# Kernel tuning notes

Hardware: AMD Instinct MI355X
Metric: run time of the kernel (lower is better)

## Reference

```python
import jax, jax.numpy as jnp
import numpy as np

PAD_IDX = 0

def _gru_layer(xs, W_ih, W_hh, b_ih, b_hh):
    # xs: [B, S, D]; W_ih: [3H, D]; W_hh: [3H, H]
    B = xs.shape[0]
    H = W_hh.shape[1]
    # precompute input-side gate projections for all timesteps: [S, B, 3H]
    xg = jnp.einsum('bsd,gd->sbg', xs, W_ih) + b_ih

    def step(h, xg_t):
        hg = h @ W_hh.T + b_hh                      # [B, 3H]
        xr, xz, xn = jnp.split(xg_t, 3, axis=-1)
        hr, hz, hn = jnp.split(hg, 3, axis=-1)
        r = jax.nn.sigmoid(xr + hr)
        z = jax.nn.sigmoid(xz + hz)
        n = jnp.tanh(xn + r * hn)
        h_new = (1.0 - z) * n + z * h
        return h_new, h_new

    h0 = jnp.zeros((B, H), dtype=xs.dtype)
    _, ys = jax.lax.scan(step, h0, xg)              # ys: [S, B, H]
    return jnp.transpose(ys, (1, 0, 2))             # [B, S, H]

def setup_inputs() -> dict:
    key = jax.random.key(0)
    ks = jax.random.split(key, 12)
    V, E, H = 32000, 256, 512
    B, S = 64, 512
    s_e = 1.0 / np.sqrt(H)
    inp = {
        'x': jax.random.randint(ks[0], (B, S), 0, V, dtype=jnp.int32),
        'emb': jax.random.normal(ks[1], (V, E), dtype=jnp.float32),
        'W_ih0': jax.random.uniform(ks[2], (3 * H, E), jnp.float32, -s_e, s_e),
        'W_hh0': jax.random.uniform(ks[3], (3 * H, H), jnp.float32, -s_e, s_e),
        'b_ih0': jax.random.uniform(ks[4], (3 * H,), jnp.float32, -s_e, s_e),
        'b_hh0': jax.random.uniform(ks[5], (3 * H,), jnp.float32, -s_e, s_e),
        'W_ih1': jax.random.uniform(ks[6], (3 * H, H), jnp.float32, -s_e, s_e),
        'W_hh1': jax.random.uniform(ks[7], (3 * H, H), jnp.float32, -s_e, s_e),
        'b_ih1': jax.random.uniform(ks[8], (3 * H,), jnp.float32, -s_e, s_e),
        'b_hh1': jax.random.uniform(ks[9], (3 * H,), jnp.float32, -s_e, s_e),
        'W_fc': jax.random.uniform(ks[10], (1, H), jnp.float32, -s_e, s_e),
        'b_fc': jax.random.uniform(ks[11], (1,), jnp.float32, -s_e, s_e),
    }
    return inp

def reference(x, emb, W_ih0, W_hh0, b_ih0, b_hh0, W_ih1, W_hh1, b_ih1, b_hh1, W_fc, b_fc):
    # embedding with padding_idx: pad row is zero
    emb_z = emb.at[PAD_IDX].set(0.0)
    h = emb_z[x]                                    # [B, S, E]
    h = _gru_layer(h, W_ih0, W_hh0, b_ih0, b_hh0)   # [B, S, H]
    h = _gru_layer(h, W_ih1, W_hh1, b_ih1, b_hh1)   # [B, S, H]
    final = h[:, -1, :]                             # [B, H]
    return jax.nn.sigmoid(final @ W_fc.T + b_fc)    # [B, 1]
```

## Files before the change

### kernel.cpp

```cpp
#include <hip/hip_runtime.h>
#include <math.h>

typedef short  s8v __attribute__((ext_vector_type(8)));
typedef float  f4v __attribute__((ext_vector_type(4)));
typedef unsigned long long ull;

#define S_LEN 512
#define BATCH 64
#define HID   512
#define TPB   256

#define WI0H_OFF 0L
#define WI0L_OFF 786432L
#define WH0H_OFF 1572864L
#define WH0L_OFF 3145728L
#define WI1H_OFF 4718592L
#define WI1L_OFF 6291456L
#define WH1H_OFF 7864320L
#define WH1L_OFF 9437184L
#define XEB_OFF  11010048L
#define H0R_OFF  27787264L
#define H1R_OFF  94896128L
#define NEED_FAST 95420416L

#define BAR_BYTES   4096
#define HBUF_BYTES  (HID*BATCH*4)
#define A_OFF       BAR_BYTES
#define B_OFF       (A_OFF + 2*HBUF_BYTES)
#define XE_OFF      (B_OFF + 2*HBUF_BYTES)
#define XE_BYTES    ((size_t)S_LEN*64*BATCH*16)

__device__ __forceinline__ float fexp2(float x){ return __builtin_amdgcn_exp2f(x); }
__device__ __forceinline__ float frcp (float x){ return __builtin_amdgcn_rcpf(x); }
__device__ __forceinline__ float sigm (float x){ return frcp(1.f + fexp2(-1.44269504089f*x)); }
__device__ __forceinline__ float tanhx(float x){ return 1.f - 2.f*frcp(1.f + fexp2(2.88539008178f*x)); }
__device__ __forceinline__ float sigmoid_f(float v){ return 1.0f/(1.0f + expf(-v)); }

__device__ __forceinline__ unsigned short f2bf(float f){
  unsigned int u = __float_as_uint(f);
  u = u + 0x7FFFu + ((u >> 16) & 1u);
  return (unsigned short)(u >> 16);
}
__device__ __forceinline__ float bf2f(unsigned short s){
  return __uint_as_float(((unsigned int)s) << 16);
}

__global__ void wcvt_kernel(const float* __restrict__ Wih0, const float* __restrict__ Whh0,
                            const float* __restrict__ Wih1, const float* __restrict__ Whh1,
                            char* __restrict__ ws)
{
  int idx = blockIdx.x * TPB + threadIdx.x;
  const float* src; long hi_off, lo_off; int pos;
  if (idx < 393216)       { src = Wih0; pos = idx;           hi_off = WI0H_OFF; lo_off = WI0L_OFF; }
  else if (idx < 1179648) { src = Whh0; pos = idx - 393216;  hi_off = WH0H_OFF; lo_off = WH0L_OFF; }
  else if (idx < 1966080) { src = Wih1; pos = idx - 1179648; hi_off = WI1H_OFF; lo_off = WI1L_OFF; }
  else                    { src = Whh1; pos = idx - 1966080; hi_off = WH1H_OFF; lo_off = WH1L_OFF; }
  float w = src[pos];
  unsigned short h = f2bf(w);
  unsigned short l = f2bf(w - bf2f(h));
  ((unsigned short*)(ws + hi_off))[pos] = h;
  ((unsigned short*)(ws + lo_off))[pos] = l;
}

__global__ void gather_xe_bf_kernel(const int* __restrict__ x,
                                    const float* __restrict__ emb,
                                    char* __restrict__ ws)
{
  int idx = blockIdx.x * TPB + threadIdx.x;
  int k4 = idx & 63;
  int n  = idx >> 6;
  int t = n >> 6, b = n & 63;
  int tok = x[b * S_LEN + t];
  float4 v = make_float4(0.f,0.f,0.f,0.f);
  if (tok != 0) v = ((const float4*)emb)[(size_t)tok * 64 + k4];
  unsigned int lo = (unsigned int)f2bf(v.x) | ((unsigned int)f2bf(v.y) << 16);
  unsigned int hi = (unsigned int)f2bf(v.z) | ((unsigned int)f2bf(v.w) << 16);
  ((uint2*)(ws + XEB_OFF))[(long)n * 64 + k4] = make_uint2(lo, hi);
}

__device__ __forceinline__ void st_rec(ull* p, ull v){
  __hip_atomic_store(p, v, __ATOMIC_RELAXED, __HIP_MEMORY_SCOPE_AGENT);
}

template<int NKS>
__device__ __forceinline__ void load_ct(const ull* __restrict__ sl, int b,
                                        int quad, int k0s, unsigned want,
                                        s8v* __restrict__ bf)
{
  ull d[NKS][4];
  for (;;){
    #pragma unroll
    for (int ks = 0; ks < NKS; ++ks){
      const int e = k0s + ks*4 + quad;
      const ull* p = sl + (long)(4*e)*64 + b;
      #pragma unroll
      for (int i = 0; i < 4; ++i)
        d[ks][i] = __hip_atomic_load(p + (long)i*64, __ATOMIC_RELAXED, __HIP_MEMORY_SCOPE_AGENT);
    }
    bool ok = true;
    #pragma unroll
    for (int ks = 0; ks < NKS; ++ks)
      #pragma unroll
      for (int i = 0; i < 4; ++i)
        ok = ok && ((unsigned)(d[ks][i] >> 32) == want);
    if (__all(ok)) break;
    __builtin_amdgcn_s_sleep(1);
  }
  #pragma unroll
  for (int ks = 0; ks < NKS; ++ks){
    s8v v;
    #pragma unroll
    for (int i = 0; i < 4; ++i){
      unsigned lo = (unsigned)d[ks][i];
      v[2*i]   = (short)(lo & 0xFFFFu);
      v[2*i+1] = (short)(lo >> 16);
    }
    bf[ks] = v;
  }
}

template<int NKS, int ROLE>
__device__ __forceinline__ void scan_body(
    int isL1, int rowWG, int bh, int wave, int lane, int tid, int j0, int b0,
    const s8v* __restrict__ Whi, const s8v* __restrict__ Wlo, int AKs, int k0s,
    const s8v* __restrict__ xsrc,
    const ull* __restrict__ rsrc, int slotMask,
    const float* __restrict__ bih, const float* __restrict__ bhh,
    ull* __restrict__ rout, int outMask,
    f4v* __restrict__ part)
{
  const int quad = lane >> 4, col = lane & 15;

  s8v ahi[3][NKS], alo[3][NKS];
  #pragma unroll
  for (int rt = 0; rt < 3; ++rt){
    const int row = rt*512 + j0 + col;
    #pragma unroll
    for (int ks = 0; ks < NKS; ++ks){
      const int e = row*AKs + k0s + ks*4 + quad;
      ahi[rt][ks] = Whi[e];
      alo[rt][ks] = Wlo[e];
    }
  }

  float cr[4], cz[4], cnx[4], cnh[4], hp[4];
  #pragma unroll
  for (int r4 = 0; r4 < 4; ++r4){
    int j = j0 + wave*4 + r4;
    cr[r4]  = bih[j]      + bhh[j];
    cz[r4]  = bih[512+j]  + bhh[512+j];
    cnx[r4] = bih[1024+j];
    cnh[r4] = bhh[1024+j];
    hp[r4]  = 0.f;
  }

  for (int t = 0; t < S_LEN; ++t){
    f4v acc[3][2];
    #pragma unroll
    for (int rt = 0; rt < 3; ++rt){ acc[rt][0] = (f4v)0.f; acc[rt][1] = (f4v)0.f; }

    const bool active = (ROLE != 1) || (t > 0);
    if (active){
      const ull* sl = (ROLE == 1) ? rsrc + (long)((t-1) & slotMask)*16384
                                  : rsrc + (long)(t & slotMask)*16384;
      const unsigned want = (ROLE == 1) ? (unsigned)t : (unsigned)(t+1);

      if (ROLE != 0){
        const ull* pp = sl + (long)(4*k0s + 4*(lane & 31) + 3)*64 + (b0 + (lane & 31));
        for (;;){
          bool pok = true;
          if (lane < 32){
            ull pv = __hip_atomic_load(pp, __ATOMIC_RELAXED, __HIP_MEMORY_SCOPE_AGENT);
            pok = ((unsigned)(pv >> 32) == want);
          }
          if (__all(pok)) break;
          __builtin_amdgcn_s_sleep(1);
        }
      }

      #pragma unroll
      for (int ct = 0; ct < 2; ++ct){
        s8v bf[NKS];
        if (ROLE == 0){
          const int nG = b0 + ct*16 + col;
          const long base = ((long)t*64 + nG)*32 + k0s + quad;
          #pragma unroll
          for (int ks = 0; ks < NKS; ++ks) bf[ks] = xsrc[base + ks*4];
        } else {
          load_ct<NKS>(sl, b0 + ct*16 + col, quad, k0s, want, bf);
        }
        #pragma unroll
        for (int ks = 0; ks < NKS; ++ks)
          #pragma unroll
          for (int rt = 0; rt < 3; ++rt){
            acc[rt][ct] = __builtin_amdgcn_mfma_f32_16x16x32_bf16(ahi[rt][ks], bf[ks], acc[rt][ct], 0, 0, 0);
            acc[rt][ct] = __builtin_amdgcn_mfma_f32_16x16x32_bf16(alo[rt][ks], bf[ks], acc[rt][ct], 0, 0, 0);
          }
      }
    }

    f4v* pb = part + (t & 1)*(4*6*64);
    #pragma unroll
    for (int rt = 0; rt < 3; ++rt)
      #pragma unroll
      for (int ct = 0; ct < 2; ++ct)
        pb[(wave*6 + rt*2 + ct)*64 + lane] = acc[rt][ct];

    asm volatile("s_waitcnt lgkmcnt(0)" ::: "memory");
    __builtin_amdgcn_s_barrier();
    asm volatile("" ::: "memory");

    if (lane < 32){
      const int b = lane;
      const int pl = wave*16 + (b & 15);
      const int ct = b >> 4;
      f4v sr = (f4v)0.f, sz = (f4v)0.f, snx = (f4v)0.f, snh = (f4v)0.f;
      #pragma unroll
      for (int w = 0; w < 4; ++w){
        const bool inpW = isL1 ? (w < 2) : (w >= 2);
        f4v g0 = pb[(w*6 + 0*2 + ct)*64 + pl];
        f4v g1 = pb[(w*6 + 1*2 + ct)*64 + pl];
        f4v g2 = pb[(w*6 + 2*2 + ct)*64 + pl];
        sr += g0; sz += g1;
        if (inpW) snx += g2; else snh += g2;
      }
      const int slotw = t & outMask;
      const ull tg = ((ull)(unsigned)(t + 1)) << 32;
      ull* ob = rout + (long)slotw*16384 + (long)(rowWG*8 + wave*2)*64 + (b0 + b);
      #pragma unroll
      for (int pr = 0; pr < 2; ++pr){
        unsigned short h2[2];
        #pragma unroll
        for (int q = 0; q < 2; ++q){
          const int r4 = pr*2 + q;
          float r = sigm(sr[r4] + cr[r4]);
          float z = sigm(sz[r4] + cz[r4]);
          float n = tanhx(snx[r4] + cnx[r4] + r*(snh[r4] + cnh[r4]));
          float h = n + z*(hp[r4] - n);
          hp[r4] = h;
          h2[q] = f2bf(h);
        }
        st_rec(ob + pr*64, ((ull)((unsigned)h2[0] | ((unsigned)h2[1] << 16))) | tg);
      }
    }
  }
}

__global__ __launch_bounds__(TPB, 1) void gru_mfma_kernel(
    const float* __restrict__ bih0, const float* __restrict__ bhh0,
    const float* __restrict__ bih1, const float* __restrict__ bhh1,
    const float* __restrict__ Wfc,  const float* __restrict__ bfc,
    float* __restrict__ out, char* __restrict__ ws)
{
  __shared__ f4v part[2*4*6*64];

  const int tid  = threadIdx.x;
  const int wg   = blockIdx.x;
  const int lane = tid & 63;
  const int wave = tid >> 6;
  const int isL1 = (wg >= 64);
  const int lw   = wg & 63;
  const int rowWG = lw >> 1;
  const int bh    = lw & 1;
  const int j0 = rowWG * 16;
  const int b0 = bh * 32;

  const s8v* wi0h = (const s8v*)(ws + WI0H_OFF); const s8v* wi0l = (const s8v*)(ws + WI0L_OFF);
  const s8v* wh0h = (const s8v*)(ws + WH0H_OFF); const s8v* wh0l = (const s8v*)(ws + WH0L_OFF);
  const s8v* wi1h = (const s8v*)(ws + WI1H_OFF); const s8v* wi1l = (const s8v*)(ws + WI1L_OFF);
  const s8v* wh1h = (const s8v*)(ws + WH1H_OFF); const s8v* wh1l = (const s8v*)(ws + WH1L_OFF);
  const s8v* xeb = (const s8v*)(ws + XEB_OFF);
  const ull* h0r = (const ull*)(ws + H0R_OFF);
  const ull* h1r = (const ull*)(ws + H1R_OFF);
  ull* h0w = (ull*)(ws + H0R_OFF);
  ull* h1w = (ull*)(ws + H1R_OFF);

  if (!isL1){
    if (wave < 2)
      scan_body<8,1>(isL1, rowWG, bh, wave, lane, tid, j0, b0,
                     wh0h, wh0l, 64, wave*32, xeb, h0r, 0x3FFFFFFF,
                     bih0, bhh0, h0w, 0x3FFFFFFF, part);
    else
      scan_body<4,0>(isL1, rowWG, bh, wave, lane, tid, j0, b0,
                     wi0h, wi0l, 32, (wave-2)*16, xeb, h0r, 0x3FFFFFFF,
                     bih0, bhh0, h0w, 0x3FFFFFFF, part);
  } else {
    if (wave < 2)
      scan_body<8,2>(isL1, rowWG, bh, wave, lane, tid, j0, b0,
                     wi1h, wi1l, 64, wave*32, xeb, h0r, 0x3FFFFFFF,
                     bih1, bhh1, h1w, 3, part);
    else
      scan_body<8,1>(isL1, rowWG, bh, wave, lane, tid, j0, b0,
                     wh1h, wh1l, 64, (wave-2)*32, xeb, h1r, 3,
                     bih1, bhh1, h1w, 3, part);
  }

  if (wg == 64 && wave == 0){
    const ull* sl = h1r + 3L*16384;
    float acc = bfc[0];
    for (int c0 = 0; c0 < 256; c0 += 32){
      ull d[32];
      for (;;){
        #pragma unroll
        for (int i = 0; i < 32; ++i)
          d[i] = __hip_atomic_load(sl + (long)(c0+i)*64 + lane,
                                   __ATOMIC_RELAXED, __HIP_MEMORY_SCOPE_AGENT);
        bool ok = true;
        #pragma unroll
        for (int i = 0; i < 32; ++i) ok = ok && ((unsigned)(d[i] >> 32) == 512u);
        if (__all(ok)) break;
        __builtin_amdgcn_s_sleep(1);
      }
      #pragma unroll
      for (int i = 0; i < 32; ++i){
        unsigned lo = (unsigned)d[i];
        int u = (c0 + i) * 2;
        acc += bf2f((unsigned short)(lo & 0xFFFFu)) * Wfc[u]
             + bf2f((unsigned short)(lo >> 16))     * Wfc[u+1];
      }
    }
    out[lane] = sigm(acc);
  }
}

__global__ void gather_xe_kernel(const int* __restrict__ x,
                                 const float* __restrict__ emb,
                                 float4* __restrict__ xe4)
{
  int idx = blockIdx.x * TPB + threadIdx.x;
  int b  = idx & 63;
  int k4 = (idx >> 6) & 63;
  int t  = idx >> 12;
  int tok = x[b * S_LEN + t];
  float4 v = make_float4(0.f, 0.f, 0.f, 0.f);
  if (tok != 0) v = ((const float4*)emb)[(size_t)tok * 64 + k4];
  xe4[idx] = v;
}

__device__ __forceinline__ void accum_vec(const float4* __restrict__ xin,
                                          const float4* __restrict__ w0,
                                          const float4* __restrict__ w1,
                                          const float4* __restrict__ w2,
                                          int n4, int lane,
                                          float& ar, float& az, float& an)
{
  #pragma unroll 4
  for (int k = 0; k < n4; ++k){
    float4 xv = xin[k * 64 + lane];
    float4 wr = w0[k], wz = w1[k], wn = w2[k];
    ar = fmaf(xv.x, wr.x, ar); az = fmaf(xv.x, wz.x, az); an = fmaf(xv.x, wn.x, an);
    ar = fmaf(xv.y, wr.y, ar); az = fmaf(xv.y, wz.y, az); an = fmaf(xv.y, wn.y, an);
    ar = fmaf(xv.z, wr.z, ar); az = fmaf(xv.z, wz.z, az); an = fmaf(xv.z, wn.z, an);
    ar = fmaf(xv.w, wr.w, ar); az = fmaf(xv.w, wz.w, az); an = fmaf(xv.w, wn.w, an);
  }
}

__device__ __forceinline__ void accum_emb(const int* __restrict__ x,
                                          const float* __restrict__ emb, int t,
                                          const float4* __restrict__ w0,
                                          const float4* __restrict__ w1,
                                          const float4* __restrict__ w2,
                                          int lane, float& ar, float& az, float& an)
{
  int tok = x[lane * S_LEN + t];
  const float4* erow = (const float4*)emb + (size_t)tok * 64;
  float m = (tok != 0) ? 1.0f : 0.0f;
  #pragma unroll 4
  for (int k = 0; k < 64; ++k){
    float4 xv = erow[k];
    float xx = xv.x*m, xy = xv.y*m, xz = xv.z*m, xw = xv.w*m;
    float4 wr = w0[k], wz = w1[k], wn = w2[k];
    ar = fmaf(xx, wr.x, ar); az = fmaf(xx, wz.x, az); an = fmaf(xx, wn.x, an);
    ar = fmaf(xy, wr.y, ar); az = fmaf(xy, wz.y, az); an = fmaf(xy, wn.y, an);
    ar = fmaf(xz, wr.z, ar); az = fmaf(xz, wz.z, az); an = fmaf(xz, wn.z, an);
    ar = fmaf(xw, wr.w, ar); az = fmaf(xw, wz.w, az); an = fmaf(xw, wn.w, an);
  }
}

__device__ __forceinline__ void stage_weights(float4* wlds, int tid, int j0, int kin4,
                                              const float* Wih, const float* Whh)
{
  const int per = 3 * (kin4 + 128);
  for (int idx = tid; idx < 4 * per; idx += TPB){
    int w = idx / per, rem = idx - w * per;
    int g = rem / (kin4 + 128), k = rem - g * (kin4 + 128);
    int row = g * HID + j0 + w;
    float4 v;
    if (k < kin4) v = ((const float4*)Wih)[(size_t)row * kin4 + k];
    else          v = ((const float4*)Whh)[(size_t)row * 128 + (k - kin4)];
    wlds[(w * 3 + g) * 256 + k] = v;
  }
}

__device__ __forceinline__ void barrier_tick(int* bar, int wg, int tid, int phase)
{
  __syncthreads();
  if (tid == 0){
    __builtin_amdgcn_fence(__ATOMIC_RELEASE, "agent");
    int* leaf = bar + 32 + (wg >> 4) * 32;
    int old = __hip_atomic_fetch_add(leaf, 1, __ATOMIC_ACQ_REL, __HIP_MEMORY_SCOPE_AGENT);
    if (old == phase * 16 + 15){
      __hip_atomic_fetch_add(bar, 1, __ATOMIC_ACQ_REL, __HIP_MEMORY_SCOPE_AGENT);
    }
    const int target = (phase + 1) * 16;
    while (__hip_atomic_load(bar, __ATOMIC_ACQUIRE, __HIP_MEMORY_SCOPE_AGENT) < target){
      __builtin_amdgcn_s_sleep(2);
    }
    __builtin_amdgcn_fence(__ATOMIC_ACQUIRE, "agent");
  }
  __syncthreads();
}

__device__ __forceinline__ void finish_store(const float4* __restrict__ hprev,
                                             float ar, float az, float anx, float anh,
                                             int lane, int j, float4* __restrict__ hout)
{
  float r  = sigmoid_f(ar);
  float zz = sigmoid_f(az);
  float n  = tanhf(fmaf(r, anh, anx));
  int fi = ((j >> 2) * 64 + lane) * 4 + (j & 3);
  float hhp = ((const float*)hprev)[fi];
  ((float*)hout)[fi] = fmaf(zz, hhp - n, n);
}

__global__ __launch_bounds__(TPB) void gru_persist_kernel(
    const int*   __restrict__ x,    const float* __restrict__ emb,
    const float* __restrict__ Wih0, const float* __restrict__ Whh0,
    const float* __restrict__ bih0, const float* __restrict__ bhh0,
    const float* __restrict__ Wih1, const float* __restrict__ Whh1,
    const float* __restrict__ bih1, const float* __restrict__ bhh1,
    const float* __restrict__ Wfc,  const float* __restrict__ bfc,
    float* __restrict__ out, int* __restrict__ bar,
    float4* __restrict__ A0, float4* __restrict__ A1,
    float4* __restrict__ B0, float4* __restrict__ B1,
    const float4* __restrict__ xe4, int use_xe)
{
  __shared__ float4 wlds[3072];
  const int tid  = threadIdx.x;
  const int wg   = blockIdx.x;
  const int lane = tid & 63;
  const int wave = tid >> 6;
  const bool isL1 = (wg >= 128);
  const int j0   = (isL1 ? wg - 128 : wg) * 4;
  const int kin4 = isL1 ? 128 : 64;

  stage_weights(wlds, tid, j0, kin4, isL1 ? Wih1 : Wih0, isL1 ? Whh1 : Whh0);
  __syncthreads();

  const int j = j0 + wave;
  const float* bih = isL1 ? bih1 : bih0;
  const float* bhh = isL1 ? bhh1 : bhh0;
  const float br  = bih[j]        + bhh[j];
  const float bz  = bih[j + 512]  + bhh[j + 512];
  const float bnx = bih[j + 1024];
  const float bnh = bhh[j + 1024];

  const float4* w0 = &wlds[(wave * 3 + 0) * 256];
  const float4* w1 = &wlds[(wave * 3 + 1) * 256];
  const float4* w2 = &wlds[(wave * 3 + 2) * 256];

  float4* A[2] = {A0, A1};
  float4* B[2] = {B0, B1};

  for (int t = 0; t <= S_LEN; ++t){
    if (!isL1){
      if (t < S_LEN){
        const float4* hprev = A[(t + 1) & 1];
        float ar = br, az = bz, anx = bnx, anh = bnh;
        if (use_xe) accum_vec(xe4 + (size_t)t * 4096, w0, w1, w2, 64, lane, ar, az, anx);
        else        accum_emb(x, emb, t, w0, w1, w2, lane, ar, az, anx);
        accum_vec(hprev, w0 + 64, w1 + 64, w2 + 64, 128, lane, ar, az, anh);
        finish_store(hprev, ar, az, anx, anh, lane, j, A[t & 1]);
      }
    } else if (t >= 1){
      const int u = t - 1;
      const float4* xin   = A[u & 1];
      const float4* hprev = B[(u + 1) & 1];
      float ar = br, az = bz, anx = bnx, anh = bnh;
      accum_vec(xin,   w0,       w1,       w2,       128, lane, ar, az, anx);
      accum_vec(hprev, w0 + 128, w1 + 128, w2 + 128, 128, lane, ar, az, anh);
      finish_store(hprev, ar, az, anx, anh, lane, j, B[u & 1]);
    }
    barrier_tick(bar, wg, tid, t);
  }

  if (wg == 0 && wave == 0){
    float acc = bfc[0];
    const float4* h1 = B[1];
    const float4* wf = (const float4*)Wfc;
    #pragma unroll 4
    for (int k = 0; k < 128; ++k){
      float4 hv = h1[k * 64 + lane];
      float4 wv = wf[k];
      acc = fmaf(hv.x, wv.x, acc); acc = fmaf(hv.y, wv.y, acc);
      acc = fmaf(hv.z, wv.z, acc); acc = fmaf(hv.w, wv.w, acc);
    }
    out[lane] = sigmoid_f(acc);
  }
}

extern "C" void kernel_launch(void* const* d_in, const int* in_sizes, int n_in,
                              void* d_out, int out_size, void* d_ws, size_t ws_size,
                              hipStream_t stream)
{
  (void)in_sizes; (void)n_in; (void)out_size;
  const int*   x    = (const int*)  d_in[0];
  const float* emb  = (const float*)d_in[1];
  const float* Wih0 = (const float*)d_in[2];
  const float* Whh0 = (const float*)d_in[3];
  const float* bih0 = (const float*)d_in[4];
  const float* bhh0 = (const float*)d_in[5];
  const float* Wih1 = (const float*)d_in[6];
  const float* Whh1 = (const float*)d_in[7];
  const float* bih1 = (const float*)d_in[8];
  const float* bhh1 = (const float*)d_in[9];
  const float* Wfc  = (const float*)d_in[10];
  const float* bfc  = (const float*)d_in[11];
  float* out = (float*)d_out;
  char* ws = (char*)d_ws;

  if (ws_size >= (size_t)NEED_FAST){
    wcvt_kernel<<<2752512 / TPB, TPB, 0, stream>>>(Wih0, Whh0, Wih1, Whh1, ws);
    gather_xe_bf_kernel<<<2097152 / TPB, TPB, 0, stream>>>(x, emb, ws);
    gru_mfma_kernel<<<128, TPB, 0, stream>>>(bih0, bhh0, bih1, bhh1, Wfc, bfc, out, ws);
  } else {
    int*    bar = (int*)ws;
    float4* A0  = (float4*)(ws + A_OFF);
    float4* A1  = (float4*)(ws + A_OFF + HBUF_BYTES);
    float4* B0  = (float4*)(ws + B_OFF);
    float4* B1  = (float4*)(ws + B_OFF + HBUF_BYTES);
    float4* xe4 = (float4*)(ws + XE_OFF);
    const int use_xe = (ws_size >= (size_t)XE_OFF + XE_BYTES) ? 1 : 0;
    hipMemsetAsync(ws, 0, XE_OFF, stream);
    if (use_xe){
      gather_xe_kernel<<<(S_LEN * 64 * BATCH) / TPB, TPB, 0, stream>>>(x, emb, xe4);
    }
    gru_persist_kernel<<<256, TPB, 0, stream>>>(
        x, emb, Wih0, Whh0, bih0, bhh0, Wih1, Whh1, bih1, bhh1, Wfc, bfc,
        out, bar, A0, A1, B0, B1, xe4, use_xe);
  }
}
```

Baseline: 2.289 ms.

## Split GRU K-dimension across all four waves for both input and hidden projections

```diff
diff --git a/kernel.cpp b/kernel.cpp
--- a/kernel.cpp
+++ b/kernel.cpp
@@ -83,63 +83,80 @@
 }
 
 template<int NKS>
-__device__ __forceinline__ void load_ct(const ull* __restrict__ sl, int b,
-                                        int quad, int k0s, unsigned want,
-                                        s8v* __restrict__ bf)
-{
-  ull d[NKS][4];
+__device__ __forceinline__ void load2(const ull* __restrict__ sl, int b0, int col,
+                                      int quad, int k0s, unsigned want,
+                                      s8v bf[2][NKS])
+{
+  ull d[2][NKS][4];
   for (;;){
     #pragma unroll
-    for (int ks = 0; ks < NKS; ++ks){
-      const int e = k0s + ks*4 + quad;
-      const ull* p = sl + (long)(4*e)*64 + b;
-      #pragma unroll
-      for (int i = 0; i < 4; ++i)
-        d[ks][i] = __hip_atomic_load(p + (long)i*64, __ATOMIC_RELAXED, __HIP_MEMORY_SCOPE_AGENT);
+    for (int ct = 0; ct < 2; ++ct){
+      const int b = b0 + ct*16 + col;
+      #pragma unroll
+      for (int ks = 0; ks < NKS; ++ks){
+        const int e = k0s + ks*4 + quad;
+        const ull* p = sl + (long)(4*e)*64 + b;
+        #pragma unroll
+        for (int i = 0; i < 4; ++i)
+          d[ct][ks][i] = __hip_atomic_load(p + (long)i*64, __ATOMIC_RELAXED, __HIP_MEMORY_SCOPE_AGENT);
+      }
     }
     bool ok = true;
     #pragma unroll
-    for (int ks = 0; ks < NKS; ++ks)
-      #pragma unroll
-      for (int i = 0; i < 4; ++i)
-        ok = ok && ((unsigned)(d[ks][i] >> 32) == want);
+    for (int ct = 0; ct < 2; ++ct)
+      #pragma unroll
+      for (int ks = 0; ks < NKS; ++ks)
+        #pragma unroll
+        for (int i = 0; i < 4; ++i)
+          ok = ok && ((unsigned)(d[ct][ks][i] >> 32) == want);
     if (__all(ok)) break;
     __builtin_amdgcn_s_sleep(1);
   }
   #pragma unroll
-  for (int ks = 0; ks < NKS; ++ks){
-    s8v v;
-    #pragma unroll
-    for (int i = 0; i < 4; ++i){
-      unsigned lo = (unsigned)d[ks][i];
-      v[2*i]   = (short)(lo & 0xFFFFu);
-      v[2*i+1] = (short)(lo >> 16);
-    }
-    bf[ks] = v;
-  }
-}
-
-template<int NKS, int ROLE>
-__device__ __forceinline__ void scan_body(
-    int isL1, int rowWG, int bh, int wave, int lane, int tid, int j0, int b0,
-    const s8v* __restrict__ Whi, const s8v* __restrict__ Wlo, int AKs, int k0s,
+  for (int ct = 0; ct < 2; ++ct)
+    #pragma unroll
+    for (int ks = 0; ks < NKS; ++ks){
+      s8v v;
+      #pragma unroll
+      for (int i = 0; i < 4; ++i){
+        unsigned lo = (unsigned)d[ct][ks][i];
+        v[2*i]   = (short)(lo & 0xFFFFu);
+        v[2*i+1] = (short)(lo >> 16);
+      }
+      bf[ct][ks] = v;
+    }
+}
+
+template<int NKSI, int TAGIN>
+__device__ __forceinline__ void scan_fused(
+    int rowWG, int wave, int lane, int j0, int b0,
+    const s8v* __restrict__ WHhi, const s8v* __restrict__ WHlo,
+    const s8v* __restrict__ WIhi, const s8v* __restrict__ WIlo,
     const s8v* __restrict__ xsrc,
-    const ull* __restrict__ rsrc, int slotMask,
+    const ull* __restrict__ rin,  int inSlotMask,
+    const ull* __restrict__ rhid, int hidSlotMask,
     const float* __restrict__ bih, const float* __restrict__ bhh,
     ull* __restrict__ rout, int outMask,
     f4v* __restrict__ part)
 {
   const int quad = lane >> 4, col = lane & 15;
-
-  s8v ahi[3][NKS], alo[3][NKS];
+  const int k0h  = wave * 16;
+  const int k0i  = wave * (NKSI * 4);
+  const int AKsI = TAGIN ? 64 : 32;
+
+  s8v hh[3][4], hl[3][4], ih[3][NKSI], il[3][NKSI];
   #pragma unroll
-  for (int rt = 0; rt < 3; ++rt){
-    const int row = rt*512 + j0 + col;
-    #pragma unroll
-    for (int ks = 0; ks < NKS; ++ks){
-      const int e = row*AKs + k0s + ks*4 + quad;
-      ahi[rt][ks] = Whi[e];
-      alo[rt][ks] = Wlo[e];
+  for (int g = 0; g < 3; ++g){
+    const int row = g*512 + j0 + col;
+    #pragma unroll
+    for (int ks = 0; ks < 4; ++ks){
+      const int e = row*64 + k0h + ks*4 + quad;
+      hh[g][ks] = WHhi[e]; hl[g][ks] = WHlo[e];
+    }
+    #pragma unroll
+    for (int ks = 0; ks < NKSI; ++ks){
+      const int e = row*AKsI + k0i + ks*4 + quad;
+      ih[g][ks] = WIhi[e]; il[g][ks] = WIlo[e];
     }
   }
 
@@ -155,56 +172,70 @@
   }
 
   for (int t = 0; t < S_LEN; ++t){
-    f4v acc[3][2];
-    #pragma unroll
-    for (int rt = 0; rt < 3; ++rt){ acc[rt][0] = (f4v)0.f; acc[rt][1] = (f4v)0.f; }
-
-    const bool active = (ROLE != 1) || (t > 0);
-    if (active){
-      const ull* sl = (ROLE == 1) ? rsrc + (long)((t-1) & slotMask)*16384
-                                  : rsrc + (long)(t & slotMask)*16384;
-      const unsigned want = (ROLE == 1) ? (unsigned)t : (unsigned)(t+1);
-
-      if (ROLE != 0){
-        const ull* pp = sl + (long)(4*k0s + 4*(lane & 31) + 3)*64 + (b0 + (lane & 31));
-        for (;;){
-          bool pok = true;
-          if (lane < 32){
-            ull pv = __hip_atomic_load(pp, __ATOMIC_RELAXED, __HIP_MEMORY_SCOPE_AGENT);
-            pok = ((unsigned)(pv >> 32) == want);
-          }
-          if (__all(pok)) break;
-          __builtin_amdgcn_s_sleep(1);
+    f4v aR[2], aZ[2], aNX[2], aNH[2];
+    #pragma unroll
+    for (int ct = 0; ct < 2; ++ct){
+      aR[ct] = (f4v)0.f; aZ[ct] = (f4v)0.f; aNX[ct] = (f4v)0.f; aNH[ct] = (f4v)0.f;
+    }
+
+    if (TAGIN == 0){
+      #pragma unroll
+      for (int ct = 0; ct < 2; ++ct){
+        const int nG = b0 + ct*16 + col;
+        const long base = ((long)t*64 + nG)*32 + k0i + quad;
+        #pragma unroll
+        for (int ks = 0; ks < NKSI; ++ks){
+          s8v bf = xsrc[base + ks*4];
+          aR[ct]  = __builtin_amdgcn_mfma_f32_16x16x32_bf16(ih[0][ks], bf, aR[ct], 0, 0, 0);
+          aR[ct]  = __builtin_amdgcn_mfma_f32_16x16x32_bf16(il[0][ks], bf, aR[ct], 0, 0, 0);
+          aZ[ct]  = __builtin_amdgcn_mfma_f32_16x16x32_bf16(ih[1][ks], bf, aZ[ct], 0, 0, 0);
+          aZ[ct]  = __builtin_amdgcn_mfma_f32_16x16x32_bf16(il[1][ks], bf, aZ[ct], 0, 0, 0);
+          aNX[ct] = __builtin_amdgcn_mfma_f32_16x16x32_bf16(ih[2][ks], bf, aNX[ct], 0, 0, 0);
+          aNX[ct] = __builtin_amdgcn_mfma_f32_16x16x32_bf16(il[2][ks], bf, aNX[ct], 0, 0, 0);
         }
       }
-
-      #pragma unroll
-      for (int ct = 0; ct < 2; ++ct){
-        s8v bf[NKS];
-        if (ROLE == 0){
-          const int nG = b0 + ct*16 + col;
-          const long base = ((long)t*64 + nG)*32 + k0s + quad;
-          #pragma unroll
-          for (int ks = 0; ks < NKS; ++ks) bf[ks] = xsrc[base + ks*4];
-        } else {
-          load_ct<NKS>(sl, b0 + ct*16 + col, quad, k0s, want, bf);
+    } else {
+      const ull* sl = rin + (long)(t & inSlotMask)*16384;
+      s8v bfi[2][NKSI];
+      load2<NKSI>(sl, b0, col, quad, k0i, (unsigned)(t+1), bfi);
+      #pragma unroll
+      for (int ct = 0; ct < 2; ++ct)
+        #pragma unroll
+        for (int ks = 0; ks < NKSI; ++ks){
+          aR[ct]  = __builtin_amdgcn_mfma_f32_16x16x32_bf16(ih[0][ks], bfi[ct][ks], aR[ct], 0, 0, 0);
+          aR[ct]  = __builtin_amdgcn_mfma_f32_16x16x32_bf16(il[0][ks], bfi[ct][ks], aR[ct], 0, 0, 0);
+          aZ[ct]  = __builtin_amdgcn_mfma_f32_16x16x32_bf16(ih[1][ks], bfi[ct][ks], aZ[ct], 0, 0, 0);
+          aZ[ct]  = __builtin_amdgcn_mfma_f32_16x16x32_bf16(il[1][ks], bfi[ct][ks], aZ[ct], 0, 0, 0);
+          aNX[ct] = __builtin_amdgcn_mfma_f32_16x16x32_bf16(ih[2][ks], bfi[ct][ks], aNX[ct], 0, 0, 0);
+          aNX[ct] = __builtin_amdgcn_mfma_f32_16x16x32_bf16(il[2][ks], bfi[ct][ks], aNX[ct], 0, 0, 0);
         }
-        #pragma unroll
-        for (int ks = 0; ks < NKS; ++ks)
-          #pragma unroll
-          for (int rt = 0; rt < 3; ++rt){
-            acc[rt][ct] = __builtin_amdgcn_mfma_f32_16x16x32_bf16(ahi[rt][ks], bf[ks], acc[rt][ct], 0, 0, 0);
-            acc[rt][ct] = __builtin_amdgcn_mfma_f32_16x16x32_bf16(alo[rt][ks], bf[ks], acc[rt][ct], 0, 0, 0);
-          }
-      }
-    }
-
-    f4v* pb = part + (t & 1)*(4*6*64);
-    #pragma unroll
-    for (int rt = 0; rt < 3; ++rt)
+    }
+
+    if (t > 0){
+      const ull* sl = rhid + (long)((t-1) & hidSlotMask)*16384;
+      s8v bfh[2][4];
+      load2<4>(sl, b0, col, quad, k0h, (unsigned)t, bfh);
       #pragma unroll
       for (int ct = 0; ct < 2; ++ct)
-        pb[(wave*6 + rt*2 + ct)*64 + lane] = acc[rt][ct];
+        #pragma unroll
+        for (int ks = 0; ks < 4; ++ks){
+          aR[ct]  = __builtin_amdgcn_mfma_f32_16x16x32_bf16(hh[0][ks], bfh[ct][ks], aR[ct], 0, 0, 0);
+          aR[ct]  = __builtin_amdgcn_mfma_f32_16x16x32_bf16(hl[0][ks], bfh[ct][ks], aR[ct], 0, 0, 0);
+          aZ[ct]  = __builtin_amdgcn_mfma_f32_16x16x32_bf16(hh[1][ks], bfh[ct][ks], aZ[ct], 0, 0, 0);
+          aZ[ct]  = __builtin_amdgcn_mfma_f32_16x16x32_bf16(hl[1][ks], bfh[ct][ks], aZ[ct], 0, 0, 0);
+          aNH[ct] = __builtin_amdgcn_mfma_f32_16x16x32_bf16(hh[2][ks], bfh[ct][ks], aNH[ct], 0, 0, 0);
+          aNH[ct] = __builtin_amdgcn_mfma_f32_16x16x32_bf16(hl[2][ks], bfh[ct][ks], aNH[ct], 0, 0, 0);
+        }
+    }
+
+    f4v* pb = part + (t & 1)*2048;
+    #pragma unroll
+    for (int ct = 0; ct < 2; ++ct){
+      pb[((wave*4 + 0)*2 + ct)*64 + lane] = aR[ct];
+      pb[((wave*4 + 1)*2 + ct)*64 + lane] = aZ[ct];
+      pb[((wave*4 + 2)*2 + ct)*64 + lane] = aNX[ct];
+      pb[((wave*4 + 3)*2 + ct)*64 + lane] = aNH[ct];
+    }
 
     asm volatile("s_waitcnt lgkmcnt(0)" ::: "memory");
     __builtin_amdgcn_s_barrier();
@@ -212,17 +243,15 @@
 
     if (lane < 32){
       const int b = lane;
+      const int ct = b >> 4;
       const int pl = wave*16 + (b & 15);
-      const int ct = b >> 4;
       f4v sr = (f4v)0.f, sz = (f4v)0.f, snx = (f4v)0.f, snh = (f4v)0.f;
       #pragma unroll
-      for (int w = 0; w < 4; ++w){
-        const bool inpW = isL1 ? (w < 2) : (w >= 2);
-        f4v g0 = pb[(w*6 + 0*2 + ct)*64 + pl];
-        f4v g1 = pb[(w*6 + 1*2 + ct)*64 + pl];
-        f4v g2 = pb[(w*6 + 2*2 + ct)*64 + pl];
-        sr += g0; sz += g1;
-        if (inpW) snx += g2; else snh += g2;
+      for (int sw = 0; sw < 4; ++sw){
+        sr  += pb[((sw*4 + 0)*2 + ct)*64 + pl];
+        sz  += pb[((sw*4 + 1)*2 + ct)*64 + pl];
+        snx += pb[((sw*4 + 2)*2 + ct)*64 + pl];
+        snh += pb[((sw*4 + 3)*2 + ct)*64 + pl];
       }
       const int slotw = t & outMask;
       const ull tg = ((ull)(unsigned)(t + 1)) << 32;
@@ -252,7 +281,7 @@
     const float* __restrict__ Wfc,  const float* __restrict__ bfc,
     float* __restrict__ out, char* __restrict__ ws)
 {
-  __shared__ f4v part[2*4*6*64];
+  __shared__ f4v part[2*2048];
 
   const int tid  = threadIdx.x;
   const int wg   = blockIdx.x;
@@ -276,23 +305,15 @@
   ull* h1w = (ull*)(ws + H1R_OFF);
 
   if (!isL1){
-    if (wave < 2)
-      scan_body<8,1>(isL1, rowWG, bh, wave, lane, tid, j0, b0,
-                     wh0h, wh0l, 64, wave*32, xeb, h0r, 0x3FFFFFFF,
-                     bih0, bhh0, h0w, 0x3FFFFFFF, part);
-    else
-      scan_body<4,0>(isL1, rowWG, bh, wave, lane, tid, j0, b0,
-                     wi0h, wi0l, 32, (wave-2)*16, xeb, h0r, 0x3FFFFFFF,
-                     bih0, bhh0, h0w, 0x3FFFFFFF, part);
+    scan_fused<2,0>(rowWG, wave, lane, j0, b0,
+                    wh0h, wh0l, wi0h, wi0l, xeb,
+                    h0r, 0, h0r, 0x3FFFFFFF,
+                    bih0, bhh0, h0w, 0x3FFFFFFF, part);
   } else {
-    if (wave < 2)
-      scan_body<8,2>(isL1, rowWG, bh, wave, lane, tid, j0, b0,
-                     wi1h, wi1l, 64, wave*32, xeb, h0r, 0x3FFFFFFF,
-                     bih1, bhh1, h1w, 3, part);
-    else
-      scan_body<8,1>(isL1, rowWG, bh, wave, lane, tid, j0, b0,
-                     wh1h, wh1l, 64, (wave-2)*32, xeb, h1r, 3,
-                     bih1, bhh1, h1w, 3, part);
+    scan_fused<4,1>(rowWG, wave, lane, j0, b0,
+                    wh1h, wh1l, wi1h, wi1l, xeb,
+                    h0r, 0x3FFFFFFF, h1r, 3,
+                    bih1, bhh1, h1w, 3, part);
   }
 
   if (wg == 64 && wave == 0){
```

New measurement: 2.095 ms. 1.09x faster.
